# Kernel tuning notes

Measured on AMD Instinct MI355X. Metric: run time of the kernel, lower is better.

The kernel has to match this reference:

```python
import jax, jax.numpy as jnp
import numpy as np

H, HK, D = 16, 4, 128          # query heads, kv heads, head_dim
HID, INTER = 2048, 8192        # hidden_size, intermediate_size
L, N_UND = 4096, 3072          # total packed len (sum(sample_lens)), num und tokens
SAMPLE_LENS = [2048, 2048]
EPS = 1e-6


def rmsnorm(x, w, eps=EPS):
    v = jnp.mean(jnp.square(x), axis=-1, keepdims=True)
    return x * jax.lax.rsqrt(v + eps) * w


def setup_inputs() -> dict:
    key = jax.random.key(0)
    ks = jax.random.split(key, 12)
    x = jax.random.normal(ks[0], (N_UND, HID), jnp.float32)
    und_idx = jnp.sort(jax.random.permutation(ks[1], L)[:N_UND]).astype(jnp.int64)
    # RoPE tables (source computes RoPE but its attention consumes pre-RoPE tensors)
    pos = jnp.arange(L, dtype=jnp.float32)
    inv_freq = 1.0 / (10000.0 ** (jnp.arange(0, D, 2, dtype=jnp.float32) / D))
    ang = pos[:, None] * inv_freq[None, :]
    cos = jnp.concatenate([jnp.cos(ang), jnp.cos(ang)], axis=-1)
    sin = jnp.concatenate([jnp.sin(ang), jnp.sin(ang)], axis=-1)
    # block-diagonal causal mask over packed sequence (one causal block per sample)
    offs = np.cumsum([0] + SAMPLE_LENS)
    m = np.zeros((L, L), dtype=bool)
    for a, b in zip(offs[:-1], offs[1:]):
        m[a:b, a:b] = np.tril(np.ones((b - a, b - a), dtype=bool))
    mask = jnp.asarray(m)
    w = lambda k, shape: jax.random.normal(k, shape, jnp.float32) * 0.02
    return dict(
        packed_sequence=x, und_idx=und_idx, cos=cos, sin=sin, mask=mask,
        Wq=w(ks[2], (H * D, HID)), bq=w(ks[3], (H * D,)),
        Wk=w(ks[4], (HK * D, HID)), bk=w(ks[5], (HK * D,)),
        Wv=w(ks[6], (HK * D, HID)), bv=w(ks[7], (HK * D,)),
        Wo=w(ks[8], (HID, H * D)),
        q_norm_w=jnp.ones((D,), jnp.float32), k_norm_w=jnp.ones((D,), jnp.float32),
        ln1_w=jnp.ones((HID,), jnp.float32), ln2_w=jnp.ones((HID,), jnp.float32),
        Wg=w(ks[9], (INTER, HID)), Wu=w(ks[10], (INTER, HID)), Wd=w(ks[11], (HID, INTER)),
    )


def reference(packed_sequence, und_idx, cos, sin, mask, Wq, bq, Wk, bk, Wv, bv, Wo,
              q_norm_w, k_norm_w, ln1_w, ln2_w, Wg, Wu, Wd):
    G = H // HK  # num_key_value_groups
    resid = packed_sequence
    x = rmsnorm(packed_sequence, ln1_w)
    # projections on und tokens only, then scatter into zero-initialized packed tensors
    q = (x @ Wq.T + bq).reshape(-1, H, D)
    k = (x @ Wk.T + bk).reshape(-1, HK, D)
    v = (x @ Wv.T + bv).reshape(-1, HK, D)
    Q = jnp.zeros((L, H, D), x.dtype).at[und_idx].set(q)
    K = jnp.zeros((L, HK, D), x.dtype).at[und_idx].set(k)
    V = jnp.zeros((L, HK, D), x.dtype).at[und_idx].set(v)
    # QK RMSNorm (zero rows stay zero, matching scatter-of-normed-und-rows)
    Q = rmsnorm(Q, q_norm_w)
    K = rmsnorm(K, k_norm_w)
    # NOTE: the source applies apply_rotary_pos_emb(Q, K, cos, sin) but both attention
    # branches consume the pre-RoPE normed tensors, so RoPE has no effect; we mirror that.
    Kx = jnp.repeat(K, G, axis=1)  # [L, H, D] GQA expand (each kv head repeated G times)
    Vx = jnp.repeat(V, G, axis=1)
    scores = jnp.einsum('qhd,khd->hqk', Q, Kx) / jnp.sqrt(jnp.asarray(D, x.dtype))
    scores = jnp.where(mask[None], scores, jnp.finfo(scores.dtype).min)
    attn = jax.nn.softmax(scores, axis=-1)
    ctx = jnp.einsum('hqk,khd->qhd', attn, Vx).reshape(L, H * D)
    attn_out = ctx[und_idx] @ Wo.T
    h = resid + attn_out
    y = rmsnorm(h, ln2_w)
    mlp = (jax.nn.silu(y @ Wg.T) * (y @ Wu.T)) @ Wd.T
    return h + mlp
```

## Files before the change

kernel.cpp:

```cpp
#include <hip/hip_runtime.h>
#include <math.h>


#define NU     3072
#define LPACK  4096
#define HIDN   2048
#define QKV_LD 3072
#define EPSF   1e-6f

typedef unsigned short u16;
typedef unsigned int   u32;
typedef __attribute__((ext_vector_type(8)))  __bf16 bf16x8;
typedef __attribute__((ext_vector_type(4)))  float  f32x4;
typedef __attribute__((ext_vector_type(16))) float  f32x16;

union FRAG { uint4 q; u16 u[8]; bf16x8 b; };

__device__ __forceinline__ u16 f2bf(float f) {
    u32 u = __float_as_uint(f);
    u32 r = (u + 0x7fffu + ((u >> 16) & 1u)) >> 16;
    return (u16)r;
}
__device__ __forceinline__ float bf2f(u16 h) {
    return __uint_as_float(((u32)h) << 16);
}
__device__ __forceinline__ void gload_lds16(const u16* g, u16* lds) {
    __builtin_amdgcn_global_load_lds(
        (const __attribute__((address_space(1))) u32*)g,
        (__attribute__((address_space(3))) u32*)lds, 16, 0, 0);
}


__global__ __launch_bounds__(256) void inv_init_kernel(int* __restrict__ inv) {
    inv[blockIdx.x * 256 + threadIdx.x] = -1;
}
__global__ __launch_bounds__(256) void inv_set_kernel(const int* __restrict__ und,
                                                      int* __restrict__ inv) {
    int i = blockIdx.x * 256 + threadIdx.x;
    inv[und[i]] = i;
}


struct CvtArgs {
    const float* src[7];
    u16*         dst[7];
    int          n8[7];
};

__global__ __launch_bounds__(256) void cvt_all_kernel(CvtArgs a) {
    int seg = blockIdx.y;
    const float* in = a.src[seg];
    u16* out = a.dst[seg];
    int n8 = a.n8[seg];
    int idx = blockIdx.x * 256 + threadIdx.x;
    int stride = gridDim.x * 256;
    for (int i = idx; i < n8; i += stride) {
        float4 va = *(const float4*)(in + (size_t)i * 8);
        float4 vb = *(const float4*)(in + (size_t)i * 8 + 4);
        FRAG f;
        f.u[0] = f2bf(va.x); f.u[1] = f2bf(va.y); f.u[2] = f2bf(va.z); f.u[3] = f2bf(va.w);
        f.u[4] = f2bf(vb.x); f.u[5] = f2bf(vb.y); f.u[6] = f2bf(vb.z); f.u[7] = f2bf(vb.w);
        *(uint4*)(out + (size_t)i * 8) = f.q;
    }
}


__global__ __launch_bounds__(256) void rmsnorm_bf16_kernel(const float* __restrict__ in,
                                                           const float* __restrict__ w,
                                                           u16* __restrict__ out) {
    int row = blockIdx.x;
    const float4* p = (const float4*)(in + (size_t)row * HIDN);
    float4 a = p[threadIdx.x * 2];
    float4 b = p[threadIdx.x * 2 + 1];
    float ss = a.x*a.x + a.y*a.y + a.z*a.z + a.w*a.w
             + b.x*b.x + b.y*b.y + b.z*b.z + b.w*b.w;
    #pragma unroll
    for (int off = 32; off > 0; off >>= 1) ss += __shfl_xor(ss, off, 64);
    __shared__ float red[4];
    if ((threadIdx.x & 63) == 0) red[threadIdx.x >> 6] = ss;
    __syncthreads();
    float tot = red[0] + red[1] + red[2] + red[3];
    float sc  = rsqrtf(tot * (1.0f / HIDN) + EPSF);
    const float4* wp = (const float4*)w;
    float4 w0 = wp[threadIdx.x * 2], w1 = wp[threadIdx.x * 2 + 1];
    FRAG f;
    f.u[0] = f2bf(a.x*sc*w0.x); f.u[1] = f2bf(a.y*sc*w0.y);
    f.u[2] = f2bf(a.z*sc*w0.z); f.u[3] = f2bf(a.w*sc*w0.w);
    f.u[4] = f2bf(b.x*sc*w1.x); f.u[5] = f2bf(b.y*sc*w1.y);
    f.u[6] = f2bf(b.z*sc*w1.z); f.u[7] = f2bf(b.w*sc*w1.w);
    *(uint4*)(out + (size_t)row * HIDN + threadIdx.x * 8) = f.q;
}


__global__ __launch_bounds__(64) void qnorm_kernel(u16* __restrict__ qkv,
                                                   const float* __restrict__ w) {
    int i = blockIdx.x, h = blockIdx.y, t = threadIdx.x;
    u16* p = qkv + (size_t)i * QKV_LD + h * 128 + t * 2;
    u32 pr = *(u32*)p;
    float x0 = bf2f((u16)(pr & 0xffff)), x1 = bf2f((u16)(pr >> 16));
    float ss = x0*x0 + x1*x1;
    #pragma unroll
    for (int off = 32; off > 0; off >>= 1) ss += __shfl_xor(ss, off, 64);
    float sc = rsqrtf(ss * (1.0f / 128.f) + EPSF);
    float2 wv = *(const float2*)(w + t * 2);
    u32 res = (u32)f2bf(x0*sc*wv.x) | ((u32)f2bf(x1*sc*wv.y) << 16);
    *(u32*)p = res;
}


__global__ __launch_bounds__(64) void scatter_kv_kernel(const u16* __restrict__ qkvb,
                                                        const int* __restrict__ inv,
                                                        const float* __restrict__ knw,
                                                        u16* __restrict__ Kb,
                                                        u16* __restrict__ Vb) {
    int l = blockIdx.x, hkk = blockIdx.y, t = threadIdx.x;
    int i = inv[l];
    size_t off = (size_t)l * 512 + hkk * 128 + t * 2;
    if (i < 0) {
        *(u32*)(Kb + off) = 0u;
        *(u32*)(Vb + off) = 0u;
        return;
    }
    const u16* kp = qkvb + (size_t)i * QKV_LD + 2048 + hkk * 128 + t * 2;
    u32 kv = *(const u32*)kp;
    float k0 = bf2f((u16)(kv & 0xffff)), k1 = bf2f((u16)(kv >> 16));
    float ss = k0*k0 + k1*k1;
    #pragma unroll
    for (int off2 = 32; off2 > 0; off2 >>= 1) ss += __shfl_xor(ss, off2, 64);
    float sc = rsqrtf(ss * (1.0f / 128.f) + EPSF);
    float2 wv = *(const float2*)(knw + t * 2);
    u32 res = (u32)f2bf(k0*sc*wv.x) | ((u32)f2bf(k1*sc*wv.y) << 16);
    *(u32*)(Kb + off) = res;
    const u16* vp = qkvb + (size_t)i * QKV_LD + 2560 + hkk * 128 + t * 2;
    *(u32*)(Vb + off) = *(const u32*)vp;
}


template <int MODE>
__global__ __launch_bounds__(256, 2) void gemm_bf16_kernel(
        const u16* __restrict__ A, int lda,
        const u16* __restrict__ B0, const u16* __restrict__ B1, const u16* __restrict__ B2,
        int n1, int n2, int ldb,
        const float* __restrict__ bias0, const float* __restrict__ bias1,
        const float* __restrict__ bias2,
        const float* __restrict__ addend,
        void* __restrict__ Cout, int ldc, int K)
{
    __shared__ u16 As[128 * 64];
    __shared__ u16 Bs[128 * 64];
    const int tid = threadIdx.x;
    const int w = tid >> 6, lane = tid & 63;
    const int m0 = blockIdx.y * 128, n0 = blockIdx.x * 128;
    const u16* Bp; const float* bias; int nb;
    if (n0 < n1)      { Bp = B0; bias = bias0; nb = n0; }
    else if (n0 < n2) { Bp = B1; bias = bias1; nb = n0 - n1; }
    else              { Bp = B2; bias = bias2; nb = n0 - n2; }
    const int wr = w >> 1, wc = w & 1;
    const int cl = lane & 15, kg = lane >> 4;

    f32x4 acc[4][4];
    #pragma unroll
    for (int i = 0; i < 4; ++i)
        #pragma unroll
        for (int j = 0; j < 4; ++j)
            #pragma unroll
            for (int r = 0; r < 4; ++r) acc[i][j][r] = 0.f;

    for (int k0 = 0; k0 < K; k0 += 64) {
        #pragma unroll
        for (int j = 0; j < 4; ++j) {
            int slot = j * 256 + tid;
            int row = slot >> 3, jp = slot & 7;
            int j2 = jp ^ (row & 7);
            gload_lds16(A + (size_t)(m0 + row) * lda + k0 + j2 * 8,
                        &As[(j * 256 + w * 64) * 8]);
        }
        #pragma unroll
        for (int j = 0; j < 4; ++j) {
            int slot = j * 256 + tid;
            int row = slot >> 3, jp = slot & 7;
            int j2 = jp ^ (row & 7);
            gload_lds16(Bp + (size_t)(nb + row) * ldb + k0 + j2 * 8,
                        &Bs[(j * 256 + w * 64) * 8]);
        }
        __syncthreads();
        #pragma unroll
        for (int ks = 0; ks < 2; ++ks) {
            FRAG af[4], bfr[4];
            #pragma unroll
            for (int mi = 0; mi < 4; ++mi) {
                int row = wr * 64 + mi * 16 + cl;
                int dblk = ks * 4 + kg;
                af[mi].q = *(const uint4*)&As[row * 64 + ((dblk ^ (row & 7)) * 8)];
            }
            #pragma unroll
            for (int ni = 0; ni < 4; ++ni) {
                int row = wc * 64 + ni * 16 + cl;
                int dblk = ks * 4 + kg;
                bfr[ni].q = *(const uint4*)&Bs[row * 64 + ((dblk ^ (row & 7)) * 8)];
            }
            #pragma unroll
            for (int mi = 0; mi < 4; ++mi)
                #pragma unroll
                for (int ni = 0; ni < 4; ++ni)
                    acc[mi][ni] = __builtin_amdgcn_mfma_f32_16x16x32_bf16(
                        af[mi].b, bfr[ni].b, acc[mi][ni], 0, 0, 0);
        }
        __syncthreads();
    }
    #pragma unroll
    for (int mi = 0; mi < 4; ++mi) {
        #pragma unroll
        for (int ni = 0; ni < 4; ++ni) {
            int gcol = n0 + wc * 64 + ni * 16 + cl;
            float bv = 0.f;
            if (MODE == 0) bv = bias[nb + wc * 64 + ni * 16 + cl];
            #pragma unroll
            for (int r = 0; r < 4; ++r) {
                int grow = m0 + wr * 64 + mi * 16 + kg * 4 + r;
                float v = acc[mi][ni][r] + bv;
                if (MODE == 0) {
                    ((u16*)Cout)[(size_t)grow * ldc + gcol] = f2bf(v);
                } else {
                    v += addend[(size_t)grow * ldc + gcol];
                    ((float*)Cout)[(size_t)grow * ldc + gcol] = v;
                }
            }
        }
    }
}


__global__ __launch_bounds__(256, 2) void gemm_gateup_bf16_kernel(
        const u16* __restrict__ A,
        const u16* __restrict__ Bg, const u16* __restrict__ Bu,
        u16* __restrict__ act, int ldc)
{
    __shared__ u16 As[128 * 64];
    __shared__ u16 Gs[128 * 64];
    __shared__ u16 Us[128 * 64];
    const int tid = threadIdx.x;
    const int w = tid >> 6, lane = tid & 63;
    const int m0 = blockIdx.y * 128, n0 = blockIdx.x * 128;
    const int wr = w >> 1, wc = w & 1;
    const int cl = lane & 15, kg = lane >> 4;

    f32x4 ag[4][4], au[4][4];
    #pragma unroll
    for (int i = 0; i < 4; ++i)
        #pragma unroll
        for (int j = 0; j < 4; ++j)
            #pragma unroll
            for (int r = 0; r < 4; ++r) { ag[i][j][r] = 0.f; au[i][j][r] = 0.f; }

    for (int k0 = 0; k0 < HIDN; k0 += 64) {
        #pragma unroll
        for (int j = 0; j < 4; ++j) {
            int slot = j * 256 + tid;
            int row = slot >> 3, jp = slot & 7;
            int j2 = jp ^ (row & 7);
            gload_lds16(A + (size_t)(m0 + row) * HIDN + k0 + j2 * 8,
                        &As[(j * 256 + w * 64) * 8]);
            gload_lds16(Bg + (size_t)(n0 + row) * HIDN + k0 + j2 * 8,
                        &Gs[(j * 256 + w * 64) * 8]);
            gload_lds16(Bu + (size_t)(n0 + row) * HIDN + k0 + j2 * 8,
                        &Us[(j * 256 + w * 64) * 8]);
        }
        __syncthreads();
        #pragma unroll
        for (int ks = 0; ks < 2; ++ks) {
            FRAG af[4], gf[4], uf[4];
            #pragma unroll
            for (int mi = 0; mi < 4; ++mi) {
                int row = wr * 64 + mi * 16 + cl;
                int dblk = ks * 4 + kg;
                af[mi].q = *(const uint4*)&As[row * 64 + ((dblk ^ (row & 7)) * 8)];
            }
            #pragma unroll
            for (int ni = 0; ni < 4; ++ni) {
                int row = wc * 64 + ni * 16 + cl;
                int dblk = ks * 4 + kg;
                gf[ni].q = *(const uint4*)&Gs[row * 64 + ((dblk ^ (row & 7)) * 8)];
                uf[ni].q = *(const uint4*)&Us[row * 64 + ((dblk ^ (row & 7)) * 8)];
            }
            #pragma unroll
            for (int mi = 0; mi < 4; ++mi)
                #pragma unroll
                for (int ni = 0; ni < 4; ++ni) {
                    ag[mi][ni] = __builtin_amdgcn_mfma_f32_16x16x32_bf16(
                        af[mi].b, gf[ni].b, ag[mi][ni], 0, 0, 0);
                    au[mi][ni] = __builtin_amdgcn_mfma_f32_16x16x32_bf16(
                        af[mi].b, uf[ni].b, au[mi][ni], 0, 0, 0);
                }
        }
        __syncthreads();
    }
    #pragma unroll
    for (int mi = 0; mi < 4; ++mi) {
        #pragma unroll
        for (int ni = 0; ni < 4; ++ni) {
            int gcol = n0 + wc * 64 + ni * 16 + cl;
            #pragma unroll
            for (int r = 0; r < 4; ++r) {
                int grow = m0 + wr * 64 + mi * 16 + kg * 4 + r;
                float g = ag[mi][ni][r], u = au[mi][ni][r];
                float s = g / (1.f + __expf(-g));
                act[(size_t)grow * ldc + gcol] = f2bf(s * u);
            }
        }
    }
}


__global__ __launch_bounds__(256, 2) void attn_mfma_kernel(
        const u16* __restrict__ qkv,
        const u16* __restrict__ Kb,
        const u16* __restrict__ Vb,
        const int* __restrict__ und,
        u16* __restrict__ ctxb)
{
    const int h = blockIdx.y, hk = h >> 2;
    const int i0 = blockIdx.x * 128;
    const int tid = threadIdx.x;
    const int w = tid >> 6, lane = tid & 63;
    const int ql = lane & 31, hi = lane >> 5;

    __shared__ __align__(16) unsigned char SM[36864];
    u16*  Kt = (u16*)SM;
    u16*  Vt = (u16*)(SM + 16384);
    float* Ot = (float*)SM;

    const int iq  = i0 + w * 32 + ql;
    const int pqv = und[iq];
    const int rsv = pqv & ~2047;
    const int kend_w = __shfl(pqv, 31, 64);
    const int kbeg_w = __shfl(pqv, 0, 64) & ~2047;
    const int kbeg_b = und[i0] & ~2047;
    const int kend_b = und[i0 + 127];
    const int nt = ((kend_b - kbeg_b) >> 5) + 1;

    FRAG qf[8];
    const u16* qbase = qkv + (size_t)iq * QKV_LD + h * 128;
    #pragma unroll
    for (int ds = 0; ds < 8; ++ds)
        qf[ds].q = *(const uint4*)(qbase + ds * 16 + hi * 8);

    f32x16 Oa[4];
    #pragma unroll
    for (int dg = 0; dg < 4; ++dg)
        #pragma unroll
        for (int r = 0; r < 16; ++r) Oa[dg][r] = 0.f;
    float m_run = -1e30f, l_run = 0.f;
    const float SCALE = 0.08838834764831845f;

    const int kp = tid & 15, d0 = (tid >> 4) * 8;

    FRAG vr0, vr1;
    {
        #pragma unroll
        for (int j = 0; j < 2; ++j) {
            int sb = (j * 4 + w) * 64;
            int slot = sb + lane;
            int r = slot >> 4, jp = slot & 15;
            int jj = jp ^ (r & 15);
            gload_lds16(Kb + (size_t)(kbeg_b + r) * 512 + hk * 128 + jj * 8,
                        &Kt[sb * 8]);
        }
        const u16* v0 = Vb + (size_t)(kbeg_b + kp * 2) * 512 + hk * 128 + d0;
        vr0.q = *(const uint4*)v0;
        vr1.q = *(const uint4*)(v0 + 512);
    }

    for (int t = 0; t < nt; ++t) {
        const int cur = t & 1;
        const int k0 = kbeg_b + t * 32;
        #pragma unroll
        for (int i = 0; i < 8; ++i) {
            u32 val = (u32)vr0.u[i] | ((u32)vr1.u[i] << 16);
            *(u32*)&Vt[cur * 5120 + (d0 + i) * 40 + kp * 2] = val;
        }
        __syncthreads();
        if (t + 1 < nt) {
            int kn = k0 + 32;
            #pragma unroll
            for (int j = 0; j < 2; ++j) {
                int sb = (j * 4 + w) * 64;
                int slot = sb + lane;
                int r = slot >> 4, jp = slot & 15;
                int jj = jp ^ (r & 15);
                gload_lds16(Kb + (size_t)(kn + r) * 512 + hk * 128 + jj * 8,
                            &Kt[(cur ^ 1) * 4096 + sb * 8]);
            }
            const u16* v0 = Vb + (size_t)(kn + kp * 2) * 512 + hk * 128 + d0;
            vr0.q = *(const uint4*)v0;
            vr1.q = *(const uint4*)(v0 + 512);
        }
        if (k0 + 31 >= kbeg_w && k0 <= kend_w) {
            f32x16 st;
            #pragma unroll
            for (int r = 0; r < 16; ++r) st[r] = 0.f;
            __builtin_amdgcn_s_setprio(1);
            #pragma unroll
            for (int ds = 0; ds < 8; ++ds) {
                FRAG kf;
                kf.q = *(const uint4*)&Kt[cur * 4096 + ql * 128 +
                                          (((ds * 2 + hi) ^ (ql & 15)) * 8)];
                st = __builtin_amdgcn_mfma_f32_32x32x16_bf16(kf.b, qf[ds].b, st, 0, 0, 0);
            }
            __builtin_amdgcn_s_setprio(0);
            float p[16];
            float mloc = -1e30f;
            #pragma unroll
            for (int r = 0; r < 16; ++r) {
                int key = k0 + (r & 3) + ((r >> 2) << 3) + (hi << 2);
                float s = (key >= rsv && key <= pqv) ? st[r] * SCALE : -1e30f;
                p[r] = s;
                mloc = fmaxf(mloc, s);
            }
            float mfull = fmaxf(mloc, __shfl_xor(mloc, 32, 64));
            float mnew = fmaxf(m_run, mfull);
            float corr = __expf(m_run - mnew);
            float psum = 0.f;
            #pragma unroll
            for (int r = 0; r < 16; ++r) {
                float e = (p[r] > -1e29f) ? __expf(p[r] - mnew) : 0.f;
                p[r] = e; psum += e;
            }
            psum += __shfl_xor(psum, 32, 64);
            l_run = l_run * corr + psum;
            if (__any(mnew > m_run)) {
                #pragma unroll
                for (int r = 0; r < 16; ++r) {
                    float cr = __shfl(corr, (r & 3) + ((r >> 2) << 3) + (hi << 2), 64);
                    #pragma unroll
                    for (int dg = 0; dg < 4; ++dg) Oa[dg][r] *= cr;
                }
            }
            m_run = mnew;
            u32 pa[2][4];
            #pragma unroll
            for (int s = 0; s < 2; ++s) {
                #pragma unroll
                for (int t2 = 0; t2 < 2; ++t2) {
                    u32 a = (u32)f2bf(p[8*s + 2*t2]) | ((u32)f2bf(p[8*s + 2*t2 + 1]) << 16);
                    u32 b = (u32)f2bf(p[8*s + 4 + 2*t2]) | ((u32)f2bf(p[8*s + 4 + 2*t2 + 1]) << 16);
                    asm volatile("v_permlane32_swap_b32 %0, %1" : "+v"(a), "+v"(b));
                    pa[s][t2] = a; pa[s][t2 + 2] = b;
                }
            }
            __builtin_amdgcn_s_setprio(1);
            #pragma unroll
            for (int s = 0; s < 2; ++s) {
                FRAG pau;
                pau.q = make_uint4(pa[s][0], pa[s][1], pa[s][2], pa[s][3]);
                #pragma unroll
                for (int dg = 0; dg < 4; ++dg) {
                    FRAG vf;
                    vf.q = *(const uint4*)&Vt[cur * 5120 + (dg * 32 + ql) * 40 +
                                              s * 16 + hi * 8];
                    Oa[dg] = __builtin_amdgcn_mfma_f32_32x32x16_bf16(pau.b, vf.b, Oa[dg], 0, 0, 0);
                }
            }
            __builtin_amdgcn_s_setprio(0);
        }
    }
    __syncthreads();

    float linv = 1.f / l_run;
    #pragma unroll
    for (int dg = 0; dg < 4; ++dg) {
        #pragma unroll
        for (int r = 0; r < 16; ++r)
            Ot[w * 1152 + ((r & 3) + ((r >> 2) << 3) + (hi << 2)) * 36 + ql] = Oa[dg][r];
        __syncthreads();
        float4 v0 = *(const float4*)&Ot[w * 1152 + ql * 36 + hi * 16 + 0];
        float4 v1 = *(const float4*)&Ot[w * 1152 + ql * 36 + hi * 16 + 4];
        float4 v2 = *(const float4*)&Ot[w * 1152 + ql * 36 + hi * 16 + 8];
        float4 v3 = *(const float4*)&Ot[w * 1152 + ql * 36 + hi * 16 + 12];
        FRAG a, b;
        a.u[0] = f2bf(v0.x * linv); a.u[1] = f2bf(v0.y * linv);
        a.u[2] = f2bf(v0.z * linv); a.u[3] = f2bf(v0.w * linv);
        a.u[4] = f2bf(v1.x * linv); a.u[5] = f2bf(v1.y * linv);
        a.u[6] = f2bf(v1.z * linv); a.u[7] = f2bf(v1.w * linv);
        b.u[0] = f2bf(v2.x * linv); b.u[1] = f2bf(v2.y * linv);
        b.u[2] = f2bf(v2.z * linv); b.u[3] = f2bf(v2.w * linv);
        b.u[4] = f2bf(v3.x * linv); b.u[5] = f2bf(v3.y * linv);
        b.u[6] = f2bf(v3.z * linv); b.u[7] = f2bf(v3.w * linv);
        u16* dst = ctxb + (size_t)(i0 + w * 32 + ql) * HIDN + h * 128 + dg * 32 + hi * 16;
        *(uint4*)dst = a.q;
        *(uint4*)(dst + 8) = b.q;
        __syncthreads();
    }
}


extern "C" void kernel_launch(void* const* d_in, const int* in_sizes, int n_in,
                              void* d_out, int out_size, void* d_ws, size_t ws_size,
                              hipStream_t stream) {
    const float* x    = (const float*)d_in[0];
    const int*   und  = (const int*)d_in[1];
    const float* Wq  = (const float*)d_in[5];
    const float* bq  = (const float*)d_in[6];
    const float* Wk  = (const float*)d_in[7];
    const float* bk  = (const float*)d_in[8];
    const float* Wv  = (const float*)d_in[9];
    const float* bv  = (const float*)d_in[10];
    const float* Wo  = (const float*)d_in[11];
    const float* qnw = (const float*)d_in[12];
    const float* knw = (const float*)d_in[13];
    const float* ln1 = (const float*)d_in[14];
    const float* ln2 = (const float*)d_in[15];
    const float* Wg  = (const float*)d_in[16];
    const float* Wu  = (const float*)d_in[17];
    const float* Wd  = (const float*)d_in[18];
    float* out = (float*)d_out;

    char* W = (char*)d_ws;
    u16* WqB = (u16*)(W + 0);
    u16* WkB = (u16*)(W + 8388608);
    u16* WvB = (u16*)(W + 10485760);
    u16* WoB = (u16*)(W + 12582912);
    u16* WgB = (u16*)(W + 20971520);
    u16* WuB = (u16*)(W + 54525952);
    u16* WdB = (u16*)(W + 88080384);
    char* R1 = W + 121634816;
    u16* qkvb = (u16*)R1;
    u16* ctxb = (u16*)(R1 + 18874368);
    u16* acth = (u16*)R1;
    float* hbuf = (float*)(W + 153092096);
    u16* xnb = (u16*)(W + 178257920);
    u16* Kbf = xnb;
    u16* Vbf = (u16*)(W + 178257920 + 4194304);
    u16* ynb = xnb;
    int* inv = (int*)(W + 190840832);

    const int BIG = 1 << 30;

    inv_init_kernel<<<16, 256, 0, stream>>>(inv);
    inv_set_kernel<<<12, 256, 0, stream>>>(und, inv);

    CvtArgs ca;
    ca.src[0] = Wq; ca.dst[0] = WqB; ca.n8[0] = 524288;
    ca.src[1] = Wk; ca.dst[1] = WkB; ca.n8[1] = 131072;
    ca.src[2] = Wv; ca.dst[2] = WvB; ca.n8[2] = 131072;
    ca.src[3] = Wo; ca.dst[3] = WoB; ca.n8[3] = 524288;
    ca.src[4] = Wg; ca.dst[4] = WgB; ca.n8[4] = 2097152;
    ca.src[5] = Wu; ca.dst[5] = WuB; ca.n8[5] = 2097152;
    ca.src[6] = Wd; ca.dst[6] = WdB; ca.n8[6] = 2097152;
    cvt_all_kernel<<<dim3(1024, 7), 256, 0, stream>>>(ca);

    rmsnorm_bf16_kernel<<<NU, 256, 0, stream>>>(x, ln1, xnb);
    gemm_bf16_kernel<0><<<dim3(24, 24), 256, 0, stream>>>(
        xnb, 2048, WqB, WkB, WvB, 2048, 2560, 2048,
        bq, bk, bv, nullptr, qkvb, QKV_LD, 2048);
    qnorm_kernel<<<dim3(NU, 16), 64, 0, stream>>>(qkvb, qnw);
    scatter_kv_kernel<<<dim3(LPACK, 4), 64, 0, stream>>>(qkvb, inv, knw, Kbf, Vbf);
    attn_mfma_kernel<<<dim3(24, 16), 256, 0, stream>>>(qkvb, Kbf, Vbf, und, ctxb);
    gemm_bf16_kernel<1><<<dim3(16, 24), 256, 0, stream>>>(
        ctxb, 2048, WoB, WoB, WoB, BIG, BIG, 2048,
        nullptr, nullptr, nullptr, x, hbuf, 2048, 2048);
    rmsnorm_bf16_kernel<<<NU, 256, 0, stream>>>(hbuf, ln2, ynb);
    gemm_gateup_bf16_kernel<<<dim3(32, 24), 256, 0, stream>>>(
        ynb, WgB, WuB, acth, 4096);
    gemm_bf16_kernel<1><<<dim3(16, 24), 256, 0, stream>>>(
        acth, 4096, WdB, WdB, WdB, BIG, BIG, 8192,
        nullptr, nullptr, nullptr, hbuf, out, 2048, 4096);
    gemm_gateup_bf16_kernel<<<dim3(32, 24), 256, 0, stream>>>(
        ynb, WgB + (size_t)4096 * 2048, WuB + (size_t)4096 * 2048, acth, 4096);
    gemm_bf16_kernel<1><<<dim3(16, 24), 256, 0, stream>>>(
        acth, 4096, WdB + 4096, WdB, WdB, BIG, BIG, 8192,
        nullptr, nullptr, nullptr, out, out, 2048, 4096);
}
```

Measured before the change: 733.2 us.

## Swizzle block order for cache locality and tighten attention softmax and V staging

The linear block IDs of the GEMM and attention kernels are remapped with a stride-8 swizzle, so consecutive blocks on the same XCD share A/B or K/V tiles in L2. In attention, the V tile's LDS row stride drops from 40 to 36 halfwords and the V fragments are read as two 64-bit loads. Softmax max and sum now use tree reductions in place, and bf16 packing uses the hardware v_cvt_pk_bf16_f32 instruction instead of manual rounding. The swizzle assumes the grid size divides evenly by 8 and hardcodes the attention grid as 24x16.

```diff
diff --git a/kernel.cpp b/kernel.cpp
--- a/kernel.cpp
+++ b/kernel.cpp
@@ -10,6 +10,7 @@
 
 typedef unsigned short u16;
 typedef unsigned int   u32;
+typedef unsigned long long u64;
 typedef __attribute__((ext_vector_type(8)))  __bf16 bf16x8;
 typedef __attribute__((ext_vector_type(4)))  float  f32x4;
 typedef __attribute__((ext_vector_type(16))) float  f32x16;
@@ -150,7 +151,11 @@
     __shared__ u16 Bs[128 * 64];
     const int tid = threadIdx.x;
     const int w = tid >> 6, lane = tid & 63;
-    const int m0 = blockIdx.y * 128, n0 = blockIdx.x * 128;
+    const int gx = gridDim.x;
+    int id = blockIdx.y * gx + blockIdx.x;
+    const int cpx = (gridDim.x * gridDim.y) >> 3;
+    id = (id & 7) * cpx + (id >> 3);
+    const int m0 = (id / gx) * 128, n0 = (id % gx) * 128;
     const u16* Bp; const float* bias; int nb;
     if (n0 < n1)      { Bp = B0; bias = bias0; nb = n0; }
     else if (n0 < n2) { Bp = B1; bias = bias1; nb = n0 - n1; }
@@ -241,7 +246,11 @@
     __shared__ u16 Us[128 * 64];
     const int tid = threadIdx.x;
     const int w = tid >> 6, lane = tid & 63;
-    const int m0 = blockIdx.y * 128, n0 = blockIdx.x * 128;
+    const int gx = gridDim.x;
+    int id = blockIdx.y * gx + blockIdx.x;
+    const int cpx = (gridDim.x * gridDim.y) >> 3;
+    id = (id & 7) * cpx + (id >> 3);
+    const int m0 = (id / gx) * 128, n0 = (id % gx) * 128;
     const int wr = w >> 1, wc = w & 1;
     const int cl = lane & 15, kg = lane >> 4;
 
@@ -319,8 +328,10 @@
         const int* __restrict__ und,
         u16* __restrict__ ctxb)
 {
-    const int h = blockIdx.y, hk = h >> 2;
-    const int i0 = blockIdx.x * 128;
+    int id = blockIdx.y * 24 + blockIdx.x;
+    id = (id & 7) * 48 + (id >> 3);
+    const int h = id / 24, hk = h >> 2;
+    const int i0 = (id % 24) * 128;
     const int tid = threadIdx.x;
     const int w = tid >> 6, lane = tid & 63;
     const int ql = lane & 31, hi = lane >> 5;
@@ -353,7 +364,7 @@
     float m_run = -1e30f, l_run = 0.f;
     const float SCALE = 0.08838834764831845f;
 
-    const int kp = tid & 15, d0 = (tid >> 4) * 8;
+    const int r2 = tid >> 4, c = tid & 15;
 
     FRAG vr0, vr1;
     {
@@ -366,7 +377,7 @@
             gload_lds16(Kb + (size_t)(kbeg_b + r) * 512 + hk * 128 + jj * 8,
                         &Kt[sb * 8]);
         }
-        const u16* v0 = Vb + (size_t)(kbeg_b + kp * 2) * 512 + hk * 128 + d0;
+        const u16* v0 = Vb + (size_t)(kbeg_b + 2 * r2) * 512 + hk * 128 + c * 8;
         vr0.q = *(const uint4*)v0;
         vr1.q = *(const uint4*)(v0 + 512);
     }
@@ -377,7 +388,7 @@
         #pragma unroll
         for (int i = 0; i < 8; ++i) {
             u32 val = (u32)vr0.u[i] | ((u32)vr1.u[i] << 16);
-            *(u32*)&Vt[cur * 5120 + (d0 + i) * 40 + kp * 2] = val;
+            *(u32*)&Vt[cur * 4608 + (c * 8 + i) * 36 + r2 * 2] = val;
         }
         __syncthreads();
         if (t + 1 < nt) {
@@ -391,7 +402,7 @@
                 gload_lds16(Kb + (size_t)(kn + r) * 512 + hk * 128 + jj * 8,
                             &Kt[(cur ^ 1) * 4096 + sb * 8]);
             }
-            const u16* v0 = Vb + (size_t)(kn + kp * 2) * 512 + hk * 128 + d0;
+            const u16* v0 = Vb + (size_t)(kn + 2 * r2) * 512 + hk * 128 + c * 8;
             vr0.q = *(const uint4*)v0;
             vr1.q = *(const uint4*)(v0 + 512);
         }
@@ -408,24 +419,28 @@
                 st = __builtin_amdgcn_mfma_f32_32x32x16_bf16(kf.b, qf[ds].b, st, 0, 0, 0);
             }
             __builtin_amdgcn_s_setprio(0);
-            float p[16];
-            float mloc = -1e30f;
+            int kh4 = k0 + (hi << 2);
             #pragma unroll
             for (int r = 0; r < 16; ++r) {
-                int key = k0 + (r & 3) + ((r >> 2) << 3) + (hi << 2);
-                float s = (key >= rsv && key <= pqv) ? st[r] * SCALE : -1e30f;
-                p[r] = s;
-                mloc = fmaxf(mloc, s);
-            }
+                int key = kh4 + (r & 3) + ((r >> 2) << 3);
+                st[r] = (key >= rsv && key <= pqv) ? st[r] * SCALE : -1e30f;
+            }
+            float ma = fmaxf(fmaxf(st[0], st[1]), fmaxf(st[2], st[3]));
+            float mb = fmaxf(fmaxf(st[4], st[5]), fmaxf(st[6], st[7]));
+            float mc = fmaxf(fmaxf(st[8], st[9]), fmaxf(st[10], st[11]));
+            float md = fmaxf(fmaxf(st[12], st[13]), fmaxf(st[14], st[15]));
+            float mloc = fmaxf(fmaxf(ma, mb), fmaxf(mc, md));
             float mfull = fmaxf(mloc, __shfl_xor(mloc, 32, 64));
             float mnew = fmaxf(m_run, mfull);
             float corr = __expf(m_run - mnew);
-            float psum = 0.f;
-            #pragma unroll
-            for (int r = 0; r < 16; ++r) {
-                float e = (p[r] > -1e29f) ? __expf(p[r] - mnew) : 0.f;
-                p[r] = e; psum += e;
-            }
+            #pragma unroll
+            for (int r = 0; r < 16; ++r)
+                st[r] = (st[r] > -1e29f) ? __expf(st[r] - mnew) : 0.f;
+            float sa = (st[0] + st[1]) + (st[2] + st[3]);
+            float sb2 = (st[4] + st[5]) + (st[6] + st[7]);
+            float sc2 = (st[8] + st[9]) + (st[10] + st[11]);
+            float sd = (st[12] + st[13]) + (st[14] + st[15]);
+            float psum = (sa + sb2) + (sc2 + sd);
             psum += __shfl_xor(psum, 32, 64);
             l_run = l_run * corr + psum;
             if (__any(mnew > m_run)) {
@@ -442,8 +457,11 @@
             for (int s = 0; s < 2; ++s) {
                 #pragma unroll
                 for (int t2 = 0; t2 < 2; ++t2) {
-                    u32 a = (u32)f2bf(p[8*s + 2*t2]) | ((u32)f2bf(p[8*s + 2*t2 + 1]) << 16);
-                    u32 b = (u32)f2bf(p[8*s + 4 + 2*t2]) | ((u32)f2bf(p[8*s + 4 + 2*t2 + 1]) << 16);
+                    u32 a, b;
+                    asm volatile("v_cvt_pk_bf16_f32 %0, %1, %2"
+                                 : "=v"(a) : "v"(st[8*s + 2*t2]), "v"(st[8*s + 2*t2 + 1]));
+                    asm volatile("v_cvt_pk_bf16_f32 %0, %1, %2"
+                                 : "=v"(b) : "v"(st[8*s + 4 + 2*t2]), "v"(st[8*s + 4 + 2*t2 + 1]));
                     asm volatile("v_permlane32_swap_b32 %0, %1" : "+v"(a), "+v"(b));
                     pa[s][t2] = a; pa[s][t2 + 2] = b;
                 }
@@ -455,10 +473,13 @@
                 pau.q = make_uint4(pa[s][0], pa[s][1], pa[s][2], pa[s][3]);
                 #pragma unroll
                 for (int dg = 0; dg < 4; ++dg) {
-                    FRAG vf;
-                    vf.q = *(const uint4*)&Vt[cur * 5120 + (dg * 32 + ql) * 40 +
-                                              s * 16 + hi * 8];
-                    Oa[dg] = __builtin_amdgcn_mfma_f32_32x32x16_bf16(pau.b, vf.b, Oa[dg], 0, 0, 0);
+                    FRAG vfr;
+                    const u16* vp = &Vt[cur * 4608 + (dg * 32 + ql) * 36 +
+                                        s * 16 + hi * 8];
+                    *(u64*)&vfr.u[0] = *(const u64*)vp;
+                    *(u64*)&vfr.u[4] = *(const u64*)(vp + 4);
+                    Oa[dg] = __builtin_amdgcn_mfma_f32_32x32x16_bf16(
+                        pau.b, vfr.b, Oa[dg], 0, 0, 0);
                 }
             }
             __builtin_amdgcn_s_setprio(0);
```

Result: faster. 704.3 us (median of 2 runs) (-3.9%).
